# Performance work log

Measured on AMD Instinct MI355X. Metric: run time of the kernel, lower is better.

The kernel has to match this reference:

```python
import jax, jax.numpy as jnp
import numpy as np

E, N = 400000, 50000
D = 128          # efeat_dim = src_dim = dst_dim = output_dim
H = 512          # hidden_dim
CAT = 3 * D      # concat of [efeat, src, dst]
LN_EPS = 1e-5


def setup_inputs() -> dict:
    key = jax.random.key(0)
    ks = jax.random.split(key, 12)
    scale = 0.02
    return {
        "efeat": jax.random.normal(ks[0], (E, D), jnp.float32),
        "src_feat": jax.random.normal(ks[1], (N, D), jnp.float32),
        "dst_feat": jax.random.normal(ks[2], (N, D), jnp.float32),
        "src_idx": jax.random.randint(ks[3], (E,), 0, N),
        "dst_idx": jax.random.randint(ks[4], (E,), 0, N),
        # MLP params: Linear(CAT,H) -> SiLU -> Linear(H,H) -> SiLU -> Linear(H,D) -> LayerNorm(D)
        "W1": jax.random.normal(ks[5], (CAT, H), jnp.float32) * scale,
        "b1": jnp.zeros((H,), jnp.float32),
        "W2": jax.random.normal(ks[6], (H, H), jnp.float32) * scale,
        "b2": jnp.zeros((H,), jnp.float32),
        "W3": jax.random.normal(ks[7], (H, D), jnp.float32) * scale,
        "b3": jnp.zeros((D,), jnp.float32),
        "gamma": jnp.ones((D,), jnp.float32),
        "beta": jnp.zeros((D,), jnp.float32),
    }


def _layer_norm(y, gamma, beta):
    mu = jnp.mean(y, axis=-1, keepdims=True)
    var = jnp.mean(jnp.square(y - mu), axis=-1, keepdims=True)
    return (y - mu) * jax.lax.rsqrt(var + LN_EPS) * gamma + beta


def reference(efeat, src_feat, dst_feat, src_idx, dst_idx,
              W1, b1, W2, b2, W3, b3, gamma, beta):
    # concat_efeat: per-edge gather of src/dst node feats + concat with edge feats
    cat = jnp.concatenate([efeat, src_feat[src_idx], dst_feat[dst_idx]], axis=1)  # [E, 3D]
    h = jax.nn.silu(cat @ W1 + b1)   # [E, H]
    h = jax.nn.silu(h @ W2 + b2)     # [E, H]
    y = h @ W3 + b3                  # [E, D]
    return _layer_norm(y, gamma, beta)
```

## Files before the change

kernel.cpp:

```cpp
#include <hip/hip_runtime.h>
#include <hip/hip_bf16.h>
#include <cstdint>
#include <cstddef>

typedef __attribute__((ext_vector_type(4))) float f32x4;
typedef __attribute__((ext_vector_type(8))) short s16x8;

#define E_ 400000
#define D_ 128
#define H_ 512
#define CAT_ 384
#define BM 64
#define NBLK 6250
#define LDS_TOTAL 65536

__device__ __forceinline__ unsigned short f2bf(float x) {
  union { float f; unsigned u; } t; t.f = x;
  return (unsigned short)((t.u + 0x8000u) >> 16);
}
__device__ __forceinline__ float silu_f(float x) {
  return x * __builtin_amdgcn_rcpf(1.0f + __expf(-x));
}

#define HS(row, byteoff) (smem + (row) * 1024 + ((byteoff) ^ (((row) & 7) << 4)))

__global__ __launch_bounds__(512, 4)
void edge_mlp_fused(const float* __restrict__ efeat,
                    const float* __restrict__ src_feat,
                    const float* __restrict__ dst_feat,
                    const int* __restrict__ src_idx,
                    const int* __restrict__ dst_idx,
                    const unsigned short* __restrict__ P1,
                    const unsigned short* __restrict__ P2,
                    const unsigned short* __restrict__ P3,
                    const float* __restrict__ b1,
                    const float* __restrict__ b2,
                    const float* __restrict__ b3,
                    const float* __restrict__ gamma,
                    const float* __restrict__ beta,
                    float* __restrict__ out) {
  extern __shared__ char smem[];
  const int tid = threadIdx.x;
  const int lane = tid & 63;
  const int wave = tid >> 6;
  const int lr = lane & 15;
  const int kc = lane >> 4;
  const int g4 = kc * 4;
  const size_t e0 = (size_t)blockIdx.x * BM;

  const unsigned short* w1base = P1 + (size_t)kc * 4096 + wave * 512 + lr * 8;
  const unsigned short* w2base = P2 + (size_t)kc * 4096 + wave * 512 + lr * 8;
  const unsigned short* w3base = P3 + (size_t)kc * 1024 + lr * 8;

  {
    const int row = tid >> 3, gq = tid & 7;
    const size_t ee = e0 + row;
    const float* bases[3];
    bases[0] = efeat + ee * D_;
    bases[1] = src_feat + (size_t)src_idx[ee] * D_;
    bases[2] = dst_feat + (size_t)dst_idx[ee] * D_;
    #pragma unroll
    for (int s = 0; s < 3; ++s) {
      #pragma unroll
      for (int i = 0; i < 2; ++i) {
        const float* sp = bases[s] + i * 64 + gq * 8;
        const f32x4 v0 = *(const f32x4*)sp;
        const f32x4 v1 = *(const f32x4*)(sp + 4);
        s16x8 w_;
        w_[0] = f2bf(v0[0]); w_[1] = f2bf(v0[1]); w_[2] = f2bf(v0[2]); w_[3] = f2bf(v0[3]);
        w_[4] = f2bf(v1[0]); w_[5] = f2bf(v1[1]); w_[6] = f2bf(v1[2]); w_[7] = f2bf(v1[3]);
        const int colb = (s * 128 + i * 64 + gq * 8) * 2;
        *(s16x8*)HS(row, colb) = w_;
      }
    }
  }
  asm volatile("s_waitcnt lgkmcnt(0)" ::: "memory");
  __builtin_amdgcn_s_barrier();
  asm volatile("" ::: "memory");

  {
    f32x4 acc[4][4];
    #pragma unroll
    for (int eg = 0; eg < 4; ++eg)
      #pragma unroll
      for (int j = 0; j < 4; ++j) acc[eg][j] = (f32x4){0.f, 0.f, 0.f, 0.f};

    #pragma unroll 2
    for (int p = 0; p < 12; ++p) {
      s16x8 w[4];
      #pragma unroll
      for (int j = 0; j < 4; ++j)
        w[j] = *(const s16x8*)(w1base + (size_t)p * 16384 + j * 128);
      #pragma unroll
      for (int eg = 0; eg < 4; ++eg) {
        const s16x8 bf = *(const s16x8*)HS(eg * 16 + lr, p * 64 + kc * 16);
        #pragma unroll
        for (int j = 0; j < 4; ++j)
          acc[eg][j] = __builtin_amdgcn_mfma_f32_16x16x32_bf16(w[j], bf, acc[eg][j], 0, 0, 0);
      }
    }

    __builtin_amdgcn_s_barrier();
    asm volatile("" ::: "memory");

    #pragma unroll
    for (int j = 0; j < 4; ++j) {
      const int col0 = (wave * 4 + j) * 16 + g4;
      const f32x4 bv = *(const f32x4*)(b1 + col0);
      #pragma unroll
      for (int eg = 0; eg < 4; ++eg) {
        ushort4 w_;
        w_.x = f2bf(silu_f(acc[eg][j][0] + bv[0]));
        w_.y = f2bf(silu_f(acc[eg][j][1] + bv[1]));
        w_.z = f2bf(silu_f(acc[eg][j][2] + bv[2]));
        w_.w = f2bf(silu_f(acc[eg][j][3] + bv[3]));
        *(ushort4*)HS(eg * 16 + lr, col0 * 2) = w_;
      }
    }
  }
  asm volatile("s_waitcnt lgkmcnt(0)" ::: "memory");
  __builtin_amdgcn_s_barrier();
  asm volatile("" ::: "memory");

  {
    f32x4 acc[4][4];
    #pragma unroll
    for (int eg = 0; eg < 4; ++eg)
      #pragma unroll
      for (int j = 0; j < 4; ++j) acc[eg][j] = (f32x4){0.f, 0.f, 0.f, 0.f};

    #pragma unroll 2
    for (int p = 0; p < 16; ++p) {
      s16x8 w[4];
      #pragma unroll
      for (int j = 0; j < 4; ++j)
        w[j] = *(const s16x8*)(w2base + (size_t)p * 16384 + j * 128);
      #pragma unroll
      for (int eg = 0; eg < 4; ++eg) {
        const s16x8 bf = *(const s16x8*)HS(eg * 16 + lr, p * 64 + kc * 16);
        #pragma unroll
        for (int j = 0; j < 4; ++j)
          acc[eg][j] = __builtin_amdgcn_mfma_f32_16x16x32_bf16(w[j], bf, acc[eg][j], 0, 0, 0);
      }
    }

    __builtin_amdgcn_s_barrier();
    asm volatile("" ::: "memory");

    #pragma unroll
    for (int j = 0; j < 4; ++j) {
      const int col0 = (wave * 4 + j) * 16 + g4;
      const f32x4 bv = *(const f32x4*)(b2 + col0);
      #pragma unroll
      for (int eg = 0; eg < 4; ++eg) {
        ushort4 w_;
        w_.x = f2bf(silu_f(acc[eg][j][0] + bv[0]));
        w_.y = f2bf(silu_f(acc[eg][j][1] + bv[1]));
        w_.z = f2bf(silu_f(acc[eg][j][2] + bv[2]));
        w_.w = f2bf(silu_f(acc[eg][j][3] + bv[3]));
        *(ushort4*)HS(eg * 16 + lr, col0 * 2) = w_;
      }
    }
  }
  asm volatile("s_waitcnt lgkmcnt(0)" ::: "memory");
  __builtin_amdgcn_s_barrier();
  asm volatile("" ::: "memory");

  if (wave < 4) {
    f32x4 acc[8];
    #pragma unroll
    for (int f = 0; f < 8; ++f) acc[f] = (f32x4){0.f, 0.f, 0.f, 0.f};

    #pragma unroll 2
    for (int p = 0; p < 16; ++p) {
      const s16x8 bf = *(const s16x8*)HS(wave * 16 + lr, p * 64 + kc * 16);
      #pragma unroll
      for (int half = 0; half < 2; ++half) {
        s16x8 w[4];
        #pragma unroll
        for (int j = 0; j < 4; ++j)
          w[j] = *(const s16x8*)(w3base + (size_t)p * 4096 + half * 512 + j * 128);
        #pragma unroll
        for (int j = 0; j < 4; ++j)
          acc[half * 4 + j] = __builtin_amdgcn_mfma_f32_16x16x32_bf16(w[j], bf, acc[half * 4 + j], 0, 0, 0);
      }
    }

    const int edge = wave * 16 + lr;
    float sum = 0.f, ss = 0.f;
    #pragma unroll
    for (int f = 0; f < 8; ++f) {
      const f32x4 bv = *(const f32x4*)(b3 + f * 16 + g4);
      #pragma unroll
      for (int r = 0; r < 4; ++r) {
        acc[f][r] += bv[r];
        sum += acc[f][r];
        ss += acc[f][r] * acc[f][r];
      }
    }
    sum += __shfl_xor(sum, 16, 64); ss += __shfl_xor(ss, 16, 64);
    sum += __shfl_xor(sum, 32, 64); ss += __shfl_xor(ss, 32, 64);
    const float mu = sum * (1.0f / 128.0f);
    const float var = ss * (1.0f / 128.0f) - mu * mu;
    const float rstd = rsqrtf(var + 1e-5f);
    float* orow = out + (e0 + edge) * D_;
    #pragma unroll
    for (int f = 0; f < 8; ++f) {
      const f32x4 gv = *(const f32x4*)(gamma + f * 16 + g4);
      const f32x4 btv = *(const f32x4*)(beta + f * 16 + g4);
      f32x4 o;
      #pragma unroll
      for (int r = 0; r < 4; ++r)
        o[r] = (acc[f][r] - mu) * rstd * gv[r] + btv[r];
      *(f32x4*)(orow + f * 16 + g4) = o;
    }
  }
}

__global__ void prep_pack(const float* __restrict__ W, unsigned short* __restrict__ P,
                          int K, int N) {
  const int t = blockIdx.x * blockDim.x + threadIdx.x;
  if (t >= N * (K >> 3)) return;
  const int n = t % N;
  const int k8 = t / N;
  const int k0 = k8 << 3;
  const int p = k0 >> 5, kc = (k0 >> 3) & 3;
  s16x8 w;
  #pragma unroll
  for (int j = 0; j < 8; ++j)
    w[j] = (short)f2bf(W[(size_t)(k0 + j) * N + n]);
  *(s16x8*)(P + (size_t)p * N * 32 + (size_t)kc * N * 8 + (size_t)n * 8) = w;
}

extern "C" void kernel_launch(void* const* d_in, const int* in_sizes, int n_in,
                              void* d_out, int out_size, void* d_ws, size_t ws_size,
                              hipStream_t stream) {
  const float* efeat    = (const float*)d_in[0];
  const float* src_feat = (const float*)d_in[1];
  const float* dst_feat = (const float*)d_in[2];
  const int*   src_idx  = (const int*)d_in[3];
  const int*   dst_idx  = (const int*)d_in[4];
  const float* W1 = (const float*)d_in[5];
  const float* b1 = (const float*)d_in[6];
  const float* W2 = (const float*)d_in[7];
  const float* b2 = (const float*)d_in[8];
  const float* W3 = (const float*)d_in[9];
  const float* b3 = (const float*)d_in[10];
  const float* gamma = (const float*)d_in[11];
  const float* beta  = (const float*)d_in[12];

  unsigned short* P1 = (unsigned short*)d_ws;
  unsigned short* P2 = P1 + 196608;
  unsigned short* P3 = P2 + 262144;

  (void)hipFuncSetAttribute((const void*)edge_mlp_fused,
                            hipFuncAttributeMaxDynamicSharedMemorySize, LDS_TOTAL);

  prep_pack<<<(512 * 48 + 255) / 256, 256, 0, stream>>>(W1, P1, CAT_, H_);
  prep_pack<<<(512 * 64 + 255) / 256, 256, 0, stream>>>(W2, P2, H_, H_);
  prep_pack<<<(128 * 64 + 255) / 256, 256, 0, stream>>>(W3, P3, H_, D_);

  edge_mlp_fused<<<NBLK, 512, LDS_TOTAL, stream>>>(
      efeat, src_feat, dst_feat, src_idx, dst_idx,
      P1, P2, P3, b1, b2, b3, gamma, beta, (float*)d_out);
}
```

Baseline: 625.5 us.

## Overlap input gathers with layer-1 MFMA, split layer-3 across all waves

Layer 1 now runs in three K-tiers. The src and dst row gathers are issued early and staged into LDS while the previous tier's MFMAs run, so gather latency is hidden behind compute. Layer 3 is split across all 8 waves, each computing half the output columns, with LayerNorm partial sums combined through a small LDS scratch area and an extra barrier. Bf16 conversion moves to the packed v_cvt_pk_bf16_f32 instruction, which changes rounding from round-half-up to the hardware mode.

Result: faster. 562.2 us (-10.1%).

```diff
diff --git a/kernel.cpp b/kernel.cpp
--- a/kernel.cpp
+++ b/kernel.cpp
@@ -5,6 +5,7 @@
 
 typedef __attribute__((ext_vector_type(4))) float f32x4;
 typedef __attribute__((ext_vector_type(8))) short s16x8;
+typedef __attribute__((ext_vector_type(4))) unsigned int u32x4;
 
 #define E_ 400000
 #define D_ 128
@@ -12,11 +13,13 @@
 #define CAT_ 384
 #define BM 64
 #define NBLK 6250
-#define LDS_TOTAL 65536
-
-__device__ __forceinline__ unsigned short f2bf(float x) {
-  union { float f; unsigned u; } t; t.f = x;
-  return (unsigned short)((t.u + 0x8000u) >> 16);
+#define SCRATCH 65536
+#define LDS_TOTAL (65536 + 1024)
+
+__device__ __forceinline__ unsigned cvtpk(float lo, float hi) {
+  unsigned r;
+  asm("v_cvt_pk_bf16_f32 %0, %1, %2" : "=v"(r) : "v"(lo), "v"(hi));
+  return r;
 }
 __device__ __forceinline__ float silu_f(float x) {
   return x * __builtin_amdgcn_rcpf(1.0f + __expf(-x));
@@ -50,27 +53,88 @@
 
   const unsigned short* w1base = P1 + (size_t)kc * 4096 + wave * 512 + lr * 8;
   const unsigned short* w2base = P2 + (size_t)kc * 4096 + wave * 512 + lr * 8;
-  const unsigned short* w3base = P3 + (size_t)kc * 1024 + lr * 8;
+
+  const int grow = tid >> 3, gq = tid & 7;
+  const size_t ee = e0 + grow;
+
+#define LOAD4(dst, base) { const float* s0_ = (base) + gq * 8; \
+  dst[0] = *(const f32x4*)s0_;        dst[1] = *(const f32x4*)(s0_ + 4); \
+  dst[2] = *(const f32x4*)(s0_ + 64); dst[3] = *(const f32x4*)(s0_ + 68); }
+
+#define STASH(v, scol) { \
+  u32x4 r0_, r1_; \
+  r0_.x = cvtpk(v[0][0], v[0][1]); r0_.y = cvtpk(v[0][2], v[0][3]); \
+  r0_.z = cvtpk(v[1][0], v[1][1]); r0_.w = cvtpk(v[1][2], v[1][3]); \
+  r1_.x = cvtpk(v[2][0], v[2][1]); r1_.y = cvtpk(v[2][2], v[2][3]); \
+  r1_.z = cvtpk(v[3][0], v[3][1]); r1_.w = cvtpk(v[3][2], v[3][3]); \
+  *(u32x4*)HS(grow, ((scol) + gq * 8) * 2) = r0_; \
+  *(u32x4*)HS(grow, ((scol) + 64 + gq * 8) * 2) = r1_; }
 
   {
-    const int row = tid >> 3, gq = tid & 7;
-    const size_t ee = e0 + row;
-    const float* bases[3];
-    bases[0] = efeat + ee * D_;
-    bases[1] = src_feat + (size_t)src_idx[ee] * D_;
-    bases[2] = dst_feat + (size_t)dst_idx[ee] * D_;
-    #pragma unroll
-    for (int s = 0; s < 3; ++s) {
-      #pragma unroll
-      for (int i = 0; i < 2; ++i) {
-        const float* sp = bases[s] + i * 64 + gq * 8;
-        const f32x4 v0 = *(const f32x4*)sp;
-        const f32x4 v1 = *(const f32x4*)(sp + 4);
-        s16x8 w_;
-        w_[0] = f2bf(v0[0]); w_[1] = f2bf(v0[1]); w_[2] = f2bf(v0[2]); w_[3] = f2bf(v0[3]);
-        w_[4] = f2bf(v1[0]); w_[5] = f2bf(v1[1]); w_[6] = f2bf(v1[2]); w_[7] = f2bf(v1[3]);
-        const int colb = (s * 128 + i * 64 + gq * 8) * 2;
-        *(s16x8*)HS(row, colb) = w_;
+    f32x4 acc[4][4];
+    #pragma unroll
+    for (int eg = 0; eg < 4; ++eg)
+      #pragma unroll
+      for (int j = 0; j < 4; ++j) acc[eg][j] = (f32x4){0.f, 0.f, 0.f, 0.f};
+
+    const float* psrc = src_feat + (size_t)src_idx[ee] * D_;
+    const float* pdst = dst_feat + (size_t)dst_idx[ee] * D_;
+
+    f32x4 gs[4], gx[4];
+    LOAD4(gs, psrc);
+    LOAD4(gx, efeat + ee * D_);
+    STASH(gx, 0);
+
+    asm volatile("s_waitcnt lgkmcnt(0)" ::: "memory");
+    __builtin_amdgcn_s_barrier();
+    asm volatile("" ::: "memory");
+
+    auto g1tier = [&](int P0) {
+      #pragma unroll
+      for (int pp = 0; pp < 4; ++pp) {
+        const int p = P0 + pp;
+        s16x8 w[4];
+        #pragma unroll
+        for (int j = 0; j < 4; ++j)
+          w[j] = *(const s16x8*)(w1base + (size_t)p * 16384 + j * 128);
+        #pragma unroll
+        for (int eg = 0; eg < 4; ++eg) {
+          const s16x8 bf = *(const s16x8*)HS(eg * 16 + lr, p * 64 + kc * 16);
+          #pragma unroll
+          for (int j = 0; j < 4; ++j)
+            acc[eg][j] = __builtin_amdgcn_mfma_f32_16x16x32_bf16(w[j], bf, acc[eg][j], 0, 0, 0);
+        }
+      }
+    };
+
+    g1tier(0);
+    STASH(gs, 128);
+    LOAD4(gx, pdst);
+    asm volatile("s_waitcnt lgkmcnt(0)" ::: "memory");
+    __builtin_amdgcn_s_barrier();
+    asm volatile("" ::: "memory");
+
+    g1tier(4);
+    STASH(gx, 256);
+    asm volatile("s_waitcnt lgkmcnt(0)" ::: "memory");
+    __builtin_amdgcn_s_barrier();
+    asm volatile("" ::: "memory");
+
+    g1tier(8);
+
+    __builtin_amdgcn_s_barrier();
+    asm volatile("" ::: "memory");
+
+    #pragma unroll
+    for (int j = 0; j < 4; ++j) {
+      const int col0 = (wave * 4 + j) * 16 + g4;
+      const f32x4 bv = *(const f32x4*)(b1 + col0);
+      #pragma unroll
+      for (int eg = 0; eg < 4; ++eg) {
+        uint2 o_;
+        o_.x = cvtpk(silu_f(acc[eg][j][0] + bv[0]), silu_f(acc[eg][j][1] + bv[1]));
+        o_.y = cvtpk(silu_f(acc[eg][j][2] + bv[2]), silu_f(acc[eg][j][3] + bv[3]));
+        *(uint2*)HS(eg * 16 + lr, col0 * 2) = o_;
       }
     }
   }
@@ -86,11 +150,11 @@
       for (int j = 0; j < 4; ++j) acc[eg][j] = (f32x4){0.f, 0.f, 0.f, 0.f};
 
     #pragma unroll 2
-    for (int p = 0; p < 12; ++p) {
+    for (int p = 0; p < 16; ++p) {
       s16x8 w[4];
       #pragma unroll
       for (int j = 0; j < 4; ++j)
-        w[j] = *(const s16x8*)(w1base + (size_t)p * 16384 + j * 128);
+        w[j] = *(const s16x8*)(w2base + (size_t)p * 16384 + j * 128);
       #pragma unroll
       for (int eg = 0; eg < 4; ++eg) {
         const s16x8 bf = *(const s16x8*)HS(eg * 16 + lr, p * 64 + kc * 16);
@@ -106,15 +170,13 @@
     #pragma unroll
     for (int j = 0; j < 4; ++j) {
       const int col0 = (wave * 4 + j) * 16 + g4;
-      const f32x4 bv = *(const f32x4*)(b1 + col0);
+      const f32x4 bv = *(const f32x4*)(b2 + col0);
       #pragma unroll
       for (int eg = 0; eg < 4; ++eg) {
-        ushort4 w_;
-        w_.x = f2bf(silu_f(acc[eg][j][0] + bv[0]));
-        w_.y = f2bf(silu_f(acc[eg][j][1] + bv[1]));
-        w_.z = f2bf(silu_f(acc[eg][j][2] + bv[2]));
-        w_.w = f2bf(silu_f(acc[eg][j][3] + bv[3]));
-        *(ushort4*)HS(eg * 16 + lr, col0 * 2) = w_;
+        uint2 o_;
+        o_.x = cvtpk(silu_f(acc[eg][j][0] + bv[0]), silu_f(acc[eg][j][1] + bv[1]));
+        o_.y = cvtpk(silu_f(acc[eg][j][2] + bv[2]), silu_f(acc[eg][j][3] + bv[3]));
+        *(uint2*)HS(eg * 16 + lr, col0 * 2) = o_;
       }
     }
   }
@@ -123,98 +185,71 @@
   asm volatile("" ::: "memory");
 
   {
-    f32x4 acc[4][4];
-    #pragma unroll
-    for (int eg = 0; eg < 4; ++eg)
-      #pragma unroll
-      for (int j = 0; j < 4; ++j) acc[eg][j] = (f32x4){0.f, 0.f, 0.f, 0.f};
+    const int eg3 = wave >> 1;
+    const int half = wave & 1;
+    const int edge = eg3 * 16 + lr;
+
+    f32x4 acc[4];
+    #pragma unroll
+    for (int j = 0; j < 4; ++j) acc[j] = (f32x4){0.f, 0.f, 0.f, 0.f};
+
+    const unsigned short* w3b = P3 + (size_t)kc * 1024 + half * 512 + lr * 8;
 
     #pragma unroll 2
     for (int p = 0; p < 16; ++p) {
       s16x8 w[4];
       #pragma unroll
       for (int j = 0; j < 4; ++j)
-        w[j] = *(const s16x8*)(w2base + (size_t)p * 16384 + j * 128);
-      #pragma unroll
-      for (int eg = 0; eg < 4; ++eg) {
-        const s16x8 bf = *(const s16x8*)HS(eg * 16 + lr, p * 64 + kc * 16);
-        #pragma unroll
-        for (int j = 0; j < 4; ++j)
-          acc[eg][j] = __builtin_amdgcn_mfma_f32_16x16x32_bf16(w[j], bf, acc[eg][j], 0, 0, 0);
-      }
-    }
-
-    __builtin_amdgcn_s_barrier();
-    asm volatile("" ::: "memory");
-
+        w[j] = *(const s16x8*)(w3b + (size_t)p * 4096 + j * 128);
+      const s16x8 bf = *(const s16x8*)HS(edge, p * 64 + kc * 16);
+      #pragma unroll
+      for (int j = 0; j < 4; ++j)
+        acc[j] = __builtin_amdgcn_mfma_f32_16x16x32_bf16(w[j], bf, acc[j], 0, 0, 0);
+    }
+
+    float sum = 0.f, ss = 0.f;
     #pragma unroll
     for (int j = 0; j < 4; ++j) {
-      const int col0 = (wave * 4 + j) * 16 + g4;
-      const f32x4 bv = *(const f32x4*)(b2 + col0);
-      #pragma unroll
-      for (int eg = 0; eg < 4; ++eg) {
-        ushort4 w_;
-        w_.x = f2bf(silu_f(acc[eg][j][0] + bv[0]));
-        w_.y = f2bf(silu_f(acc[eg][j][1] + bv[1]));
-        w_.z = f2bf(silu_f(acc[eg][j][2] + bv[2]));
-        w_.w = f2bf(silu_f(acc[eg][j][3] + bv[3]));
-        *(ushort4*)HS(eg * 16 + lr, col0 * 2) = w_;
-      }
-    }
-  }
-  asm volatile("s_waitcnt lgkmcnt(0)" ::: "memory");
-  __builtin_amdgcn_s_barrier();
-  asm volatile("" ::: "memory");
-
-  if (wave < 4) {
-    f32x4 acc[8];
-    #pragma unroll
-    for (int f = 0; f < 8; ++f) acc[f] = (f32x4){0.f, 0.f, 0.f, 0.f};
-
-    #pragma unroll 2
-    for (int p = 0; p < 16; ++p) {
-      const s16x8 bf = *(const s16x8*)HS(wave * 16 + lr, p * 64 + kc * 16);
-      #pragma unroll
-      for (int half = 0; half < 2; ++half) {
-        s16x8 w[4];
-        #pragma unroll
-        for (int j = 0; j < 4; ++j)
-          w[j] = *(const s16x8*)(w3base + (size_t)p * 4096 + half * 512 + j * 128);
-        #pragma unroll
-        for (int j = 0; j < 4; ++j)
-          acc[half * 4 + j] = __builtin_amdgcn_mfma_f32_16x16x32_bf16(w[j], bf, acc[half * 4 + j], 0, 0, 0);
-      }
-    }
-
-    const int edge = wave * 16 + lr;
-    float sum = 0.f, ss = 0.f;
-    #pragma unroll
-    for (int f = 0; f < 8; ++f) {
-      const f32x4 bv = *(const f32x4*)(b3 + f * 16 + g4);
+      const f32x4 bv = *(const f32x4*)(b3 + half * 64 + j * 16 + g4);
       #pragma unroll
       for (int r = 0; r < 4; ++r) {
-        acc[f][r] += bv[r];
-        sum += acc[f][r];
-        ss += acc[f][r] * acc[f][r];
+        acc[j][r] += bv[r];
+        sum += acc[j][r];
+        ss += acc[j][r] * acc[j][r];
       }
     }
     sum += __shfl_xor(sum, 16, 64); ss += __shfl_xor(ss, 16, 64);
     sum += __shfl_xor(sum, 32, 64); ss += __shfl_xor(ss, 32, 64);
-    const float mu = sum * (1.0f / 128.0f);
-    const float var = ss * (1.0f / 128.0f) - mu * mu;
+
+    if (lane < 16) {
+      float2 pw; pw.x = sum; pw.y = ss;
+      *(float2*)(smem + SCRATCH + edge * 16 + half * 8) = pw;
+    }
+    asm volatile("s_waitcnt lgkmcnt(0)" ::: "memory");
+    __builtin_amdgcn_s_barrier();
+    asm volatile("" ::: "memory");
+
+    const f32x4 pt = *(const f32x4*)(smem + SCRATCH + edge * 16);
+    const float sumT = pt[0] + pt[2];
+    const float ssT  = pt[1] + pt[3];
+    const float mu = sumT * (1.0f / 128.0f);
+    const float var = ssT * (1.0f / 128.0f) - mu * mu;
     const float rstd = rsqrtf(var + 1e-5f);
-    float* orow = out + (e0 + edge) * D_;
-    #pragma unroll
-    for (int f = 0; f < 8; ++f) {
-      const f32x4 gv = *(const f32x4*)(gamma + f * 16 + g4);
-      const f32x4 btv = *(const f32x4*)(beta + f * 16 + g4);
+
+    float* orow = out + (e0 + edge) * D_ + half * 64;
+    #pragma unroll
+    for (int j = 0; j < 4; ++j) {
+      const f32x4 gv  = *(const f32x4*)(gamma + half * 64 + j * 16 + g4);
+      const f32x4 btv = *(const f32x4*)(beta  + half * 64 + j * 16 + g4);
       f32x4 o;
       #pragma unroll
       for (int r = 0; r < 4; ++r)
-        o[r] = (acc[f][r] - mu) * rstd * gv[r] + btv[r];
-      *(f32x4*)(orow + f * 16 + g4) = o;
+        o[r] = (acc[j][r] - mu) * rstd * gv[r] + btv[r];
+      *(f32x4*)(orow + j * 16 + g4) = o;
     }
   }
+#undef LOAD4
+#undef STASH
 }
 
 __global__ void prep_pack(const float* __restrict__ W, unsigned short* __restrict__ P,
@@ -227,8 +262,10 @@
   const int p = k0 >> 5, kc = (k0 >> 3) & 3;
   s16x8 w;
   #pragma unroll
-  for (int j = 0; j < 8; ++j)
-    w[j] = (short)f2bf(W[(size_t)(k0 + j) * N + n]);
+  for (int j = 0; j < 8; ++j) {
+    union { float f; unsigned u; } t_; t_.f = W[(size_t)(k0 + j) * N + n];
+    w[j] = (short)((t_.u + 0x8000u) >> 16);
+  }
   *(s16x8*)(P + (size_t)p * N * 32 + (size_t)kc * N * 8 + (size_t)n * 8) = w;
 }
 
```
